# Performance work log

Measured on AMD Instinct MI355X. Metric: run time of the kernel, lower is better.

## Reference

```python
import jax, jax.numpy as jnp
import numpy as np

B, C, HEADS, W, Hh = 8, 512, 8, 32, 32
D = C // HEADS  # 64 per-head dim
N = W * Hh      # 1024 spatial tokens


def setup_inputs() -> dict:
    key = jax.random.key(0)
    ks = jax.random.split(key, 10)
    s = 1.0 / np.sqrt(C)
    return {
        "x": jax.random.normal(ks[0], (B, C, W, Hh), dtype=jnp.float32),
        "Wq": jax.random.normal(ks[1], (C, C), dtype=jnp.float32) * s,
        "bq": jax.random.normal(ks[2], (C,), dtype=jnp.float32) * 0.01,
        "Wk": jax.random.normal(ks[3], (C, C), dtype=jnp.float32) * s,
        "bk": jax.random.normal(ks[4], (C,), dtype=jnp.float32) * 0.01,
        "Wv": jax.random.normal(ks[5], (C, C), dtype=jnp.float32) * s,
        "bv": jax.random.normal(ks[6], (C,), dtype=jnp.float32) * 0.01,
        "rel_h": jax.random.normal(ks[7], (1, HEADS, D, 1, Hh), dtype=jnp.float32),
        "rel_w": jax.random.normal(ks[8], (1, HEADS, D, W, 1), dtype=jnp.float32),
    }


def reference(x, Wq, bq, Wk, bk, Wv, bv, rel_h, rel_w):
    b = x.shape[0]
    xf = x.reshape(b, C, N)  # [B, C, N] — 1x1 conv == per-position linear
    proj = lambda Wm, bm: (jnp.einsum('oc,bcn->bon', Wm, xf) + bm[None, :, None]).reshape(b, HEADS, D, N)
    q = proj(Wq, bq)  # [B, H, D, N]
    k = proj(Wk, bk)
    v = proj(Wv, bv)
    # content-content: q^T k -> [B, H, N, N]
    cc = jnp.einsum('bhdn,bhdm->bhnm', q, k)
    # relative position bias: (rel_h + rel_w) -> [H, D, N], then rel^T @ q
    rel = (rel_h + rel_w).reshape(HEADS, D, N)
    cp = jnp.einsum('hdn,bhdm->bhnm', rel, q)  # [B, H, N, N]
    attn = jax.nn.softmax(cc + cp, axis=-1)
    # out = v @ attn^T : out[d,m] = sum_n v[d,n] * attn[m,n]
    out = jnp.einsum('bhdn,bhmn->bhdm', v, attn)  # [B, H, D, N]
    return out.reshape(b, C, W, Hh)
```

## Files before the change

kernel.cpp:

```cpp
#include <hip/hip_runtime.h>

typedef _Float16 half8 __attribute__((ext_vector_type(8)));
typedef _Float16 half4 __attribute__((ext_vector_type(4)));
typedef float f32x4 __attribute__((ext_vector_type(4)));

__device__ __forceinline__ void glds16(const void* g, void* l) {
    __builtin_amdgcn_global_load_lds(
        (const __attribute__((address_space(1))) unsigned int*)g,
        (__attribute__((address_space(3))) unsigned int*)l, 16, 0, 0);
}


__global__ void k_prep_all(const float* __restrict__ Wq, const float* __restrict__ Wk,
                           const float* __restrict__ Wv, const float* __restrict__ bq,
                           const float* __restrict__ bk, const float* __restrict__ bv,
                           const float* __restrict__ x, const float* __restrict__ rel_h,
                           const float* __restrict__ rel_w, _Float16* __restrict__ Wf,
                           float* __restrict__ bias2, _Float16* __restrict__ xTf,
                           _Float16* __restrict__ rel2) {
    __shared__ float xs[64][65];
    int bid = blockIdx.x;
    if (bid < 384) {
        int t = bid * 256 + threadIdx.x;
        int m = t >> 6;
        int c8 = (t & 63) << 3;
        const float* src = (m < 512) ? (Wq + m * 512)
                         : (m < 1024 ? (Wk + (m - 512) * 512) : (Wv + (m - 1024) * 512));
        float4 v0 = *(const float4*)(src + c8);
        float4 v1 = *(const float4*)(src + c8 + 4);
        half8 o;
        o[0] = (_Float16)v0.x; o[1] = (_Float16)v0.y; o[2] = (_Float16)v0.z; o[3] = (_Float16)v0.w;
        o[4] = (_Float16)v1.x; o[5] = (_Float16)v1.y; o[6] = (_Float16)v1.z; o[7] = (_Float16)v1.w;
        *(half8*)(Wf + (size_t)m * 512 + c8) = o;
        if (t < 1536)
            bias2[t] = (t < 512) ? bq[t] : (t < 1024 ? bk[t - 512] : bv[t - 1024]);
    } else if (bid < 1408) {
        int i = bid - 384;
        int nt = (i & 15) << 6, ct = ((i >> 4) & 7) << 6, b = i >> 7;
        int t = threadIdx.x;
        const float* xb = x + ((size_t)b * 512 + ct) * 1024 + nt;
#pragma unroll
        for (int p = 0; p < 4; ++p) {
            int c = p * 16 + (t >> 4), n4 = (t & 15) * 4;
            float4 v = *(const float4*)(xb + (size_t)c * 1024 + n4);
            xs[c][n4] = v.x; xs[c][n4 + 1] = v.y; xs[c][n4 + 2] = v.z; xs[c][n4 + 3] = v.w;
        }
        __syncthreads();
        int nl = t >> 2, part = t & 3;
        _Float16* rowp = xTf + ((size_t)b * 1024 + nt + nl) * 512;
#pragma unroll
        for (int g = 0; g < 2; ++g) {
            half8 o;
#pragma unroll
            for (int j = 0; j < 8; ++j)
                o[j] = (_Float16)xs[part * 16 + g * 8 + j][nl];
            *(half8*)(rowp + ct + part * 16 + g * 8) = o;
        }
    } else {
        int tid = (bid - 1408) * 256 + threadIdx.x;
        int h = tid >> 13;
        int rem = tid & 8191;
        int n = rem >> 3;
        int g = rem & 7;
        int hh = n & 31, ww = n >> 5;
        half8 o;
#pragma unroll
        for (int j = 0; j < 8; ++j) {
            int d = g * 8 + j;
            o[j] = (_Float16)(rel_h[(h * 64 + d) * 32 + hh] + rel_w[(h * 64 + d) * 32 + ww]);
        }
        *(half8*)(rel2 + ((size_t)h * 1024 + n) * 64 + g * 8) = o;
    }
}

__global__ __launch_bounds__(256, 3) void k_proj(const _Float16* __restrict__ Wf,
                                                 const _Float16* __restrict__ xTf,
                                                 const float* __restrict__ bias2,
                                                 _Float16* __restrict__ q2,
                                                 _Float16* __restrict__ k2,
                                                 _Float16* __restrict__ vb) {
    __shared__ __align__(16) _Float16 As[8192];
    __shared__ __align__(16) _Float16 Bs[8192];
    int t = threadIdx.x;
    int lane = t & 63, w = t >> 6;
    int lm = lane & 15, lq = lane >> 4;
    int wr = (w >> 1) * 64, wc = (w & 1) * 64;
    int mb = blockIdx.y * 128, nb = blockIdx.x * 128, b = blockIdx.z;
    int rl = lane >> 2;
    int csw = ((lane & 3) ^ ((lane >> 3) & 3)) * 8;
    const _Float16* Ag0 = Wf + (size_t)(mb + w * 32 + rl) * 512 + csw;
    const _Float16* Ag1 = Ag0 + 16 * 512;
    const _Float16* Bg0 = xTf + ((size_t)b * 1024 + nb + w * 32 + rl) * 512 + csw;
    const _Float16* Bg1 = Bg0 + 16 * 512;
    f32x4 acc[4][4];
#pragma unroll
    for (int i = 0; i < 4; ++i)
#pragma unroll
        for (int j = 0; j < 4; ++j) acc[i][j] = {0.f, 0.f, 0.f, 0.f};
    int fsw = (lq ^ ((lm >> 1) & 3)) * 8;
    for (int k0 = 0; k0 < 512; k0 += 64) {
#pragma unroll
        for (int kh = 0; kh < 2; ++kh) {
            int ko = k0 + kh * 32;
            glds16(Ag0 + ko, &As[kh * 4096 + (w * 32) * 32]);
            glds16(Ag1 + ko, &As[kh * 4096 + (w * 32 + 16) * 32]);
            glds16(Bg0 + ko, &Bs[kh * 4096 + (w * 32) * 32]);
            glds16(Bg1 + ko, &Bs[kh * 4096 + (w * 32 + 16) * 32]);
        }
        __syncthreads();
#pragma unroll
        for (int kh = 0; kh < 2; ++kh) {
            half8 af[4], bfr[4];
#pragma unroll
            for (int mt = 0; mt < 4; ++mt)
                af[mt] = *(half8*)&As[kh * 4096 + (wr + mt * 16 + lm) * 32 + fsw];
#pragma unroll
            for (int nt = 0; nt < 4; ++nt)
                bfr[nt] = *(half8*)&Bs[kh * 4096 + (wc + nt * 16 + lm) * 32 + fsw];
#pragma unroll
            for (int mt = 0; mt < 4; ++mt)
#pragma unroll
                for (int nt = 0; nt < 4; ++nt)
                    acc[mt][nt] = __builtin_amdgcn_mfma_f32_16x16x32_f16(af[mt], bfr[nt], acc[mt][nt], 0, 0, 0);
        }
        __syncthreads();
    }
    int sect = mb >> 9;
    int hloc = ((mb & 511) + wr) >> 6;
    size_t bh = (size_t)b * 8 + hloc;
    if (sect < 2) {
        float sc = (sect == 0) ? 1.44269504089f : 1.0f;
        _Float16* dst = (sect == 0 ? q2 : k2) + bh * 1024 * 64;
#pragma unroll
        for (int mt = 0; mt < 4; ++mt) {
            int d0 = mt * 16 + lq * 4;
            float bi0 = bias2[mb + wr + d0];
            float bi1 = bias2[mb + wr + d0 + 1];
            float bi2 = bias2[mb + wr + d0 + 2];
            float bi3 = bias2[mb + wr + d0 + 3];
#pragma unroll
            for (int nt = 0; nt < 4; ++nt) {
                int n = nb + wc + nt * 16 + lm;
                half4 o;
                o[0] = (_Float16)((acc[mt][nt][0] + bi0) * sc);
                o[1] = (_Float16)((acc[mt][nt][1] + bi1) * sc);
                o[2] = (_Float16)((acc[mt][nt][2] + bi2) * sc);
                o[3] = (_Float16)((acc[mt][nt][3] + bi3) * sc);
                *(half4*)(dst + (size_t)n * 64 + d0) = o;
            }
        }
    } else {
        _Float16* dst = vb + bh * 64 * 1024;
#pragma unroll
        for (int mt = 0; mt < 4; ++mt)
#pragma unroll
            for (int reg = 0; reg < 4; ++reg) {
                int d = mt * 16 + lq * 4 + reg;
                float bi = bias2[mb + wr + d];
#pragma unroll
                for (int nt = 0; nt < 4; ++nt) {
                    int n = nb + wc + nt * 16 + lm;
                    dst[(size_t)d * 1024 + n] = (_Float16)(acc[mt][nt][reg] + bi);
                }
            }
    }
}

__global__ __launch_bounds__(256, 3) void k_attn(const _Float16* __restrict__ q2,
                                                 const _Float16* __restrict__ k2,
                                                 const _Float16* __restrict__ rel2,
                                                 const _Float16* __restrict__ vb,
                                                 float* __restrict__ out) {
    __shared__ __align__(16) char pool[45056];
    _Float16* kb_s = (_Float16*)pool;
    _Float16* v_s  = (_Float16*)(pool + 17408);
    _Float16* p_s  = (_Float16*)(pool + 26624);
    int t = threadIdx.x;
    int lane = t & 63, w = t >> 6;
    int lm = lane & 15, lq = lane >> 4;
    int lin = blockIdx.x;
    int mt0 = lin >> 6;
    int bh_ = lin & 63;
    int h = bh_ & 7, b = bh_ >> 3;
    size_t bh = (size_t)b * 8 + h;
    const _Float16* q2b = q2 + bh * 1024 * 64;
    const _Float16* k2b = k2 + bh * 1024 * 64;
    const _Float16* relb = rel2 + (size_t)h * 1024 * 64;
    const _Float16* vbb = vb + bh * 64 * 1024;
    float* outb = out + bh * 64 * 1024 + mt0 * 128;

    int r = t >> 2, part = t & 3;
    const _Float16* ksrc = ((part < 2) ? (k2b + part * 32) : (q2b + (part - 2) * 32));
    int vc = (t & 3) * 16;
    const _Float16* vsrcb = vbb + (size_t)r * 1024 + vc;
    _Float16* kdst = kb_s + r * 136 + part * 32;
    _Float16* vdst = v_s + r * 72 + vc;

    uint4 kc0, kc1, kc2, kc3, vv0, vv1;
    {
        const uint4* s_ = (const uint4*)(ksrc + (size_t)r * 64);
        kc0 = s_[0]; kc1 = s_[1]; kc2 = s_[2]; kc3 = s_[3];
        const uint4* v_ = (const uint4*)vsrcb;
        vv0 = v_[0]; vv1 = v_[1];
    }

    {
        int n = mt0 * 128 + r;
        const _Float16* src = (part < 2) ? (q2b + (size_t)n * 64 + part * 32)
                                         : (relb + (size_t)n * 64 + (part - 2) * 32);
        ((uint4*)kdst)[0] = ((const uint4*)src)[0];
        ((uint4*)kdst)[1] = ((const uint4*)src)[1];
        ((uint4*)kdst)[2] = ((const uint4*)src)[2];
        ((uint4*)kdst)[3] = ((const uint4*)src)[3];
    }
    __syncthreads();
    half8 ah0[4], ah1[4];
#pragma unroll
    for (int kk = 0; kk < 4; ++kk)
        ah0[kk] = *(half8*)&kb_s[(w * 16 + lm) * 136 + kk * 32 + lq * 8];
    __syncthreads();
    {
        int n = mt0 * 128 + 64 + r;
        const _Float16* src = (part < 2) ? (q2b + (size_t)n * 64 + part * 32)
                                         : (relb + (size_t)n * 64 + (part - 2) * 32);
        ((uint4*)kdst)[0] = ((const uint4*)src)[0];
        ((uint4*)kdst)[1] = ((const uint4*)src)[1];
        ((uint4*)kdst)[2] = ((const uint4*)src)[2];
        ((uint4*)kdst)[3] = ((const uint4*)src)[3];
    }
    __syncthreads();
#pragma unroll
    for (int kk = 0; kk < 4; ++kk)
        ah1[kk] = *(half8*)&kb_s[(w * 16 + lm) * 136 + kk * 32 + lq * 8];
    __syncthreads();

    f32x4 acco0[4], acco1[4];
#pragma unroll
    for (int i = 0; i < 4; ++i) { acco0[i] = {0.f, 0.f, 0.f, 0.f}; acco1[i] = {0.f, 0.f, 0.f, 0.f}; }
    float mrun0 = -3e38f, lrun0 = 0.f, mrun1 = -3e38f, lrun1 = 0.f;

    for (int kt = 0; kt < 16; ++kt) {
        ((uint4*)kdst)[0] = kc0;
        ((uint4*)kdst)[1] = kc1;
        ((uint4*)kdst)[2] = kc2;
        ((uint4*)kdst)[3] = kc3;
        ((uint4*)vdst)[0] = vv0;
        ((uint4*)vdst)[1] = vv1;
        __syncthreads();
        int nn = ((kt + 1) & 15) * 64;
        const uint4* s_ = (const uint4*)(ksrc + (size_t)(nn + r) * 64);
        uint4 kn0 = s_[0], kn1 = s_[1], kn2 = s_[2], kn3 = s_[3];
        const uint4* v_ = (const uint4*)(vsrcb + nn);
        uint4 vn0 = v_[0], vn1 = v_[1];
        f32x4 s0[4], s1[4];
#pragma unroll
        for (int ct = 0; ct < 4; ++ct) { s0[ct] = {0.f, 0.f, 0.f, 0.f}; s1[ct] = {0.f, 0.f, 0.f, 0.f}; }
#pragma unroll
        for (int ct = 0; ct < 4; ++ct) {
            half8 kf[4];
#pragma unroll
            for (int kk = 0; kk < 4; ++kk)
                kf[kk] = *(half8*)&kb_s[(ct * 16 + lm) * 136 + kk * 32 + lq * 8];
#pragma unroll
            for (int kk = 0; kk < 4; ++kk) {
                s0[ct] = __builtin_amdgcn_mfma_f32_16x16x32_f16(kf[kk], ah0[kk], s0[ct], 0, 0, 0);
                s1[ct] = __builtin_amdgcn_mfma_f32_16x16x32_f16(kf[kk], ah1[kk], s1[ct], 0, 0, 0);
            }
        }
        {
            float mx = -3e38f;
#pragma unroll
            for (int ct = 0; ct < 4; ++ct)
#pragma unroll
                for (int reg = 0; reg < 4; ++reg) mx = fmaxf(mx, s0[ct][reg]);
            mx = fmaxf(mx, __shfl_xor(mx, 16));
            mx = fmaxf(mx, __shfl_xor(mx, 32));
            float mnew = fmaxf(mrun0, mx);
            float al_ = exp2f(mrun0 - mnew);
            float rs = 0.f;
#pragma unroll
            for (int ct = 0; ct < 4; ++ct) {
                float p0 = exp2f(s0[ct][0] - mnew);
                float p1 = exp2f(s0[ct][1] - mnew);
                float p2 = exp2f(s0[ct][2] - mnew);
                float p3 = exp2f(s0[ct][3] - mnew);
                rs += (p0 + p1) + (p2 + p3);
                half4 o; o[0] = (_Float16)p0; o[1] = (_Float16)p1; o[2] = (_Float16)p2; o[3] = (_Float16)p3;
                *(half4*)&p_s[(w * 16 + lm) * 72 + ct * 16 + lq * 4] = o;
            }
            rs += __shfl_xor(rs, 16);
            rs += __shfl_xor(rs, 32);
            lrun0 = lrun0 * al_ + rs;
            mrun0 = mnew;
#pragma unroll
            for (int dt = 0; dt < 4; ++dt) {
                acco0[dt][0] *= al_; acco0[dt][1] *= al_;
                acco0[dt][2] *= al_; acco0[dt][3] *= al_;
            }
        }
        {
            float mx = -3e38f;
#pragma unroll
            for (int ct = 0; ct < 4; ++ct)
#pragma unroll
                for (int reg = 0; reg < 4; ++reg) mx = fmaxf(mx, s1[ct][reg]);
            mx = fmaxf(mx, __shfl_xor(mx, 16));
            mx = fmaxf(mx, __shfl_xor(mx, 32));
            float mnew = fmaxf(mrun1, mx);
            float al_ = exp2f(mrun1 - mnew);
            float rs = 0.f;
#pragma unroll
            for (int ct = 0; ct < 4; ++ct) {
                float p0 = exp2f(s1[ct][0] - mnew);
                float p1 = exp2f(s1[ct][1] - mnew);
                float p2 = exp2f(s1[ct][2] - mnew);
                float p3 = exp2f(s1[ct][3] - mnew);
                rs += (p0 + p1) + (p2 + p3);
                half4 o; o[0] = (_Float16)p0; o[1] = (_Float16)p1; o[2] = (_Float16)p2; o[3] = (_Float16)p3;
                *(half4*)&p_s[(64 + w * 16 + lm) * 72 + ct * 16 + lq * 4] = o;
            }
            rs += __shfl_xor(rs, 16);
            rs += __shfl_xor(rs, 32);
            lrun1 = lrun1 * al_ + rs;
            mrun1 = mnew;
#pragma unroll
            for (int dt = 0; dt < 4; ++dt) {
                acco1[dt][0] *= al_; acco1[dt][1] *= al_;
                acco1[dt][2] *= al_; acco1[dt][3] *= al_;
            }
        }
        half8 p0f[2], p1f[2];
#pragma unroll
        for (int ch = 0; ch < 2; ++ch) {
            p0f[ch] = *(half8*)&p_s[(w * 16 + lm) * 72 + ch * 32 + lq * 8];
            p1f[ch] = *(half8*)&p_s[(64 + w * 16 + lm) * 72 + ch * 32 + lq * 8];
        }
#pragma unroll
        for (int dt = 0; dt < 4; ++dt) {
            half8 vf0 = *(half8*)&v_s[(dt * 16 + lm) * 72 + lq * 8];
            half8 vf1 = *(half8*)&v_s[(dt * 16 + lm) * 72 + 32 + lq * 8];
            acco0[dt] = __builtin_amdgcn_mfma_f32_16x16x32_f16(vf0, p0f[0], acco0[dt], 0, 0, 0);
            acco0[dt] = __builtin_amdgcn_mfma_f32_16x16x32_f16(vf1, p0f[1], acco0[dt], 0, 0, 0);
            acco1[dt] = __builtin_amdgcn_mfma_f32_16x16x32_f16(vf0, p1f[0], acco1[dt], 0, 0, 0);
            acco1[dt] = __builtin_amdgcn_mfma_f32_16x16x32_f16(vf1, p1f[1], acco1[dt], 0, 0, 0);
        }
        __syncthreads();
        kc0 = kn0; kc1 = kn1; kc2 = kn2; kc3 = kn3;
        vv0 = vn0; vv1 = vn1;
    }
    float li0 = 1.f / lrun0, li1 = 1.f / lrun1;
#pragma unroll
    for (int dt = 0; dt < 4; ++dt)
#pragma unroll
        for (int reg = 0; reg < 4; ++reg) {
            int d = dt * 16 + lq * 4 + reg;
            outb[(size_t)d * 1024 + w * 16 + lm] = acco0[dt][reg] * li0;
            outb[(size_t)d * 1024 + 64 + w * 16 + lm] = acco1[dt][reg] * li1;
        }
}

extern "C" void kernel_launch(void* const* d_in, const int* in_sizes, int n_in,
                              void* d_out, int out_size, void* d_ws, size_t ws_size,
                              hipStream_t stream) {
    const float* x     = (const float*)d_in[0];
    const float* Wq    = (const float*)d_in[1];
    const float* bq    = (const float*)d_in[2];
    const float* Wk    = (const float*)d_in[3];
    const float* bk    = (const float*)d_in[4];
    const float* Wv    = (const float*)d_in[5];
    const float* bv    = (const float*)d_in[6];
    const float* rel_h = (const float*)d_in[7];
    const float* rel_w = (const float*)d_in[8];
    char* ws = (char*)d_ws;
    _Float16* Wf   = (_Float16*)(ws);
    float* bias2   = (float*)(ws + 1572864);
    _Float16* xTf  = (_Float16*)(ws + 1579008);
    _Float16* q2   = (_Float16*)(ws + 9967616);
    _Float16* k2   = (_Float16*)(ws + 18356224);
    _Float16* vb   = (_Float16*)(ws + 26744832);
    _Float16* rel2 = (_Float16*)(ws + 35133440);
    float* out = (float*)d_out;

    hipLaunchKernelGGL(k_prep_all, dim3(1664),     dim3(256), 0, stream,
                       Wq, Wk, Wv, bq, bk, bv, x, rel_h, rel_w, Wf, bias2, xTf, rel2);
    hipLaunchKernelGGL(k_proj,     dim3(8, 12, 8), dim3(256), 0, stream, Wf, xTf, bias2, q2, k2, vb);
    hipLaunchKernelGGL(k_attn,     dim3(512),      dim3(256), 0, stream, q2, k2, rel2, vb, out);
}
```

Baseline: 153.6 us.

## Swizzle attention LDS tiles, add lazy softmax rescale, setprio and packed conversion

Replaces the padded LDS layouts for the K/Q, V and P tiles with XOR-swizzled unpadded rows, aiming to avoid bank conflicts while shrinking shared memory. Online softmax now rescales the accumulators only when the row max grows by more than a threshold, which skips most rescale multiplies. MFMA sections are wrapped in s_setprio, and probabilities are converted with the packed round-toward-zero instruction. The lazy rescale lets unnormalised values grow up to 2^8 before rescaling, which is a small fp16 precision and overflow risk.

```diff
diff --git a/kernel.cpp b/kernel.cpp
--- a/kernel.cpp
+++ b/kernel.cpp
@@ -2,6 +2,7 @@
 
 typedef _Float16 half8 __attribute__((ext_vector_type(8)));
 typedef _Float16 half4 __attribute__((ext_vector_type(4)));
+typedef __fp16 fp16x2 __attribute__((ext_vector_type(2)));
 typedef float f32x4 __attribute__((ext_vector_type(4)));
 
 __device__ __forceinline__ void glds16(const void* g, void* l) {
@@ -171,10 +172,10 @@
                                                  const _Float16* __restrict__ rel2,
                                                  const _Float16* __restrict__ vb,
                                                  float* __restrict__ out) {
-    __shared__ __align__(16) char pool[45056];
-    _Float16* kb_s = (_Float16*)pool;
-    _Float16* v_s  = (_Float16*)(pool + 17408);
-    _Float16* p_s  = (_Float16*)(pool + 26624);
+    __shared__ __align__(16) char pool[40960];
+    char* kb_s = pool;
+    char* v_s  = pool + 16384;
+    char* p_s  = pool + 24576;
     int t = threadIdx.x;
     int lane = t & 63, w = t >> 6;
     int lm = lane & 15, lq = lane >> 4;
@@ -190,11 +191,12 @@
     float* outb = out + bh * 64 * 1024 + mt0 * 128;
 
     int r = t >> 2, part = t & 3;
+    int wsw = (r & 7) << 4;
+    int rsw = (lm & 7) << 4;
     const _Float16* ksrc = ((part < 2) ? (k2b + part * 32) : (q2b + (part - 2) * 32));
-    int vc = (t & 3) * 16;
-    const _Float16* vsrcb = vbb + (size_t)r * 1024 + vc;
-    _Float16* kdst = kb_s + r * 136 + part * 32;
-    _Float16* vdst = v_s + r * 72 + vc;
+    const _Float16* vsrcb = vbb + (size_t)r * 1024 + part * 16;
+    char* kdst = kb_s + r * 256;
+    char* vdst = v_s + r * 128;
 
     uint4 kc0, kc1, kc2, kc3, vv0, vv1;
     {
@@ -208,30 +210,30 @@
         int n = mt0 * 128 + r;
         const _Float16* src = (part < 2) ? (q2b + (size_t)n * 64 + part * 32)
                                          : (relb + (size_t)n * 64 + (part - 2) * 32);
-        ((uint4*)kdst)[0] = ((const uint4*)src)[0];
-        ((uint4*)kdst)[1] = ((const uint4*)src)[1];
-        ((uint4*)kdst)[2] = ((const uint4*)src)[2];
-        ((uint4*)kdst)[3] = ((const uint4*)src)[3];
+        *(uint4*)(kdst + ((part * 64 +  0) ^ wsw)) = ((const uint4*)src)[0];
+        *(uint4*)(kdst + ((part * 64 + 16) ^ wsw)) = ((const uint4*)src)[1];
+        *(uint4*)(kdst + ((part * 64 + 32) ^ wsw)) = ((const uint4*)src)[2];
+        *(uint4*)(kdst + ((part * 64 + 48) ^ wsw)) = ((const uint4*)src)[3];
     }
     __syncthreads();
     half8 ah0[4], ah1[4];
 #pragma unroll
     for (int kk = 0; kk < 4; ++kk)
-        ah0[kk] = *(half8*)&kb_s[(w * 16 + lm) * 136 + kk * 32 + lq * 8];
+        ah0[kk] = *(half8*)(kb_s + (w * 16 + lm) * 256 + ((kk * 64 + lq * 16) ^ rsw));
     __syncthreads();
     {
         int n = mt0 * 128 + 64 + r;
         const _Float16* src = (part < 2) ? (q2b + (size_t)n * 64 + part * 32)
                                          : (relb + (size_t)n * 64 + (part - 2) * 32);
-        ((uint4*)kdst)[0] = ((const uint4*)src)[0];
-        ((uint4*)kdst)[1] = ((const uint4*)src)[1];
-        ((uint4*)kdst)[2] = ((const uint4*)src)[2];
-        ((uint4*)kdst)[3] = ((const uint4*)src)[3];
+        *(uint4*)(kdst + ((part * 64 +  0) ^ wsw)) = ((const uint4*)src)[0];
+        *(uint4*)(kdst + ((part * 64 + 16) ^ wsw)) = ((const uint4*)src)[1];
+        *(uint4*)(kdst + ((part * 64 + 32) ^ wsw)) = ((const uint4*)src)[2];
+        *(uint4*)(kdst + ((part * 64 + 48) ^ wsw)) = ((const uint4*)src)[3];
     }
     __syncthreads();
 #pragma unroll
     for (int kk = 0; kk < 4; ++kk)
-        ah1[kk] = *(half8*)&kb_s[(w * 16 + lm) * 136 + kk * 32 + lq * 8];
+        ah1[kk] = *(half8*)(kb_s + (w * 16 + lm) * 256 + ((kk * 64 + lq * 16) ^ rsw));
     __syncthreads();
 
     f32x4 acco0[4], acco1[4];
@@ -240,12 +242,12 @@
     float mrun0 = -3e38f, lrun0 = 0.f, mrun1 = -3e38f, lrun1 = 0.f;
 
     for (int kt = 0; kt < 16; ++kt) {
-        ((uint4*)kdst)[0] = kc0;
-        ((uint4*)kdst)[1] = kc1;
-        ((uint4*)kdst)[2] = kc2;
-        ((uint4*)kdst)[3] = kc3;
-        ((uint4*)vdst)[0] = vv0;
-        ((uint4*)vdst)[1] = vv1;
+        *(uint4*)(kdst + ((part * 64 +  0) ^ wsw)) = kc0;
+        *(uint4*)(kdst + ((part * 64 + 16) ^ wsw)) = kc1;
+        *(uint4*)(kdst + ((part * 64 + 32) ^ wsw)) = kc2;
+        *(uint4*)(kdst + ((part * 64 + 48) ^ wsw)) = kc3;
+        *(uint4*)(vdst + ((part * 32 +  0) ^ wsw)) = vv0;
+        *(uint4*)(vdst + ((part * 32 + 16) ^ wsw)) = vv1;
         __syncthreads();
         int nn = ((kt + 1) & 15) * 64;
         const uint4* s_ = (const uint4*)(ksrc + (size_t)(nn + r) * 64);
@@ -255,95 +257,119 @@
         f32x4 s0[4], s1[4];
 #pragma unroll
         for (int ct = 0; ct < 4; ++ct) { s0[ct] = {0.f, 0.f, 0.f, 0.f}; s1[ct] = {0.f, 0.f, 0.f, 0.f}; }
+        __builtin_amdgcn_s_setprio(1);
 #pragma unroll
         for (int ct = 0; ct < 4; ++ct) {
             half8 kf[4];
 #pragma unroll
             for (int kk = 0; kk < 4; ++kk)
-                kf[kk] = *(half8*)&kb_s[(ct * 16 + lm) * 136 + kk * 32 + lq * 8];
+                kf[kk] = *(half8*)(kb_s + (ct * 16 + lm) * 256 + ((kk * 64 + lq * 16) ^ rsw));
 #pragma unroll
             for (int kk = 0; kk < 4; ++kk) {
                 s0[ct] = __builtin_amdgcn_mfma_f32_16x16x32_f16(kf[kk], ah0[kk], s0[ct], 0, 0, 0);
                 s1[ct] = __builtin_amdgcn_mfma_f32_16x16x32_f16(kf[kk], ah1[kk], s1[ct], 0, 0, 0);
             }
         }
+        __builtin_amdgcn_s_setprio(0);
         {
             float mx = -3e38f;
 #pragma unroll
-            for (int ct = 0; ct < 4; ++ct)
-#pragma unroll
-                for (int reg = 0; reg < 4; ++reg) mx = fmaxf(mx, s0[ct][reg]);
+            for (int ct = 0; ct < 4; ++ct) {
+                float a_ = fmaxf(s0[ct][0], s0[ct][1]);
+                float b2 = fmaxf(s0[ct][2], s0[ct][3]);
+                mx = fmaxf(mx, fmaxf(a_, b2));
+            }
             mx = fmaxf(mx, __shfl_xor(mx, 16));
             mx = fmaxf(mx, __shfl_xor(mx, 32));
-            float mnew = fmaxf(mrun0, mx);
-            float al_ = exp2f(mrun0 - mnew);
+            if (__any(mx > mrun0 + 8.f)) {
+                float mnew = fmaxf(mrun0, mx);
+                float al_ = exp2f(mrun0 - mnew);
+                lrun0 *= al_;
+#pragma unroll
+                for (int dt = 0; dt < 4; ++dt) {
+                    acco0[dt][0] *= al_; acco0[dt][1] *= al_;
+                    acco0[dt][2] *= al_; acco0[dt][3] *= al_;
+                }
+                mrun0 = mnew;
+            }
             float rs = 0.f;
+            char* prow = p_s + (w * 16 + lm) * 128;
 #pragma unroll
             for (int ct = 0; ct < 4; ++ct) {
-                float p0 = exp2f(s0[ct][0] - mnew);
-                float p1 = exp2f(s0[ct][1] - mnew);
-                float p2 = exp2f(s0[ct][2] - mnew);
-                float p3 = exp2f(s0[ct][3] - mnew);
+                float p0 = exp2f(s0[ct][0] - mrun0);
+                float p1 = exp2f(s0[ct][1] - mrun0);
+                float p2 = exp2f(s0[ct][2] - mrun0);
+                float p3 = exp2f(s0[ct][3] - mrun0);
                 rs += (p0 + p1) + (p2 + p3);
-                half4 o; o[0] = (_Float16)p0; o[1] = (_Float16)p1; o[2] = (_Float16)p2; o[3] = (_Float16)p3;
-                *(half4*)&p_s[(w * 16 + lm) * 72 + ct * 16 + lq * 4] = o;
+                fp16x2 lo = __builtin_amdgcn_cvt_pkrtz(p0, p1);
+                fp16x2 hi = __builtin_amdgcn_cvt_pkrtz(p2, p3);
+                uint2 pk;
+                pk.x = __builtin_bit_cast(unsigned int, lo);
+                pk.y = __builtin_bit_cast(unsigned int, hi);
+                *(uint2*)(prow + ((ct * 32 + lq * 8) ^ rsw)) = pk;
             }
             rs += __shfl_xor(rs, 16);
             rs += __shfl_xor(rs, 32);
-            lrun0 = lrun0 * al_ + rs;
-            mrun0 = mnew;
-#pragma unroll
-            for (int dt = 0; dt < 4; ++dt) {
-                acco0[dt][0] *= al_; acco0[dt][1] *= al_;
-                acco0[dt][2] *= al_; acco0[dt][3] *= al_;
-            }
+            lrun0 += rs;
         }
         {
             float mx = -3e38f;
 #pragma unroll
-            for (int ct = 0; ct < 4; ++ct)
-#pragma unroll
-                for (int reg = 0; reg < 4; ++reg) mx = fmaxf(mx, s1[ct][reg]);
+            for (int ct = 0; ct < 4; ++ct) {
+                float a_ = fmaxf(s1[ct][0], s1[ct][1]);
+                float b2 = fmaxf(s1[ct][2], s1[ct][3]);
+                mx = fmaxf(mx, fmaxf(a_, b2));
+            }
             mx = fmaxf(mx, __shfl_xor(mx, 16));
             mx = fmaxf(mx, __shfl_xor(mx, 32));
-            float mnew = fmaxf(mrun1, mx);
-            float al_ = exp2f(mrun1 - mnew);
+            if (__any(mx > mrun1 + 8.f)) {
+                float mnew = fmaxf(mrun1, mx);
+                float al_ = exp2f(mrun1 - mnew);
+                lrun1 *= al_;
+#pragma unroll
+                for (int dt = 0; dt < 4; ++dt) {
+                    acco1[dt][0] *= al_; acco1[dt][1] *= al_;
+                    acco1[dt][2] *= al_; acco1[dt][3] *= al_;
+                }
+                mrun1 = mnew;
+            }
             float rs = 0.f;
+            char* prow = p_s + (64 + w * 16 + lm) * 128;
 #pragma unroll
             for (int ct = 0; ct < 4; ++ct) {
-                float p0 = exp2f(s1[ct][0] - mnew);
-                float p1 = exp2f(s1[ct][1] - mnew);
-                float p2 = exp2f(s1[ct][2] - mnew);
-                float p3 = exp2f(s1[ct][3] - mnew);
+                float p0 = exp2f(s1[ct][0] - mrun1);
+                float p1 = exp2f(s1[ct][1] - mrun1);
+                float p2 = exp2f(s1[ct][2] - mrun1);
+                float p3 = exp2f(s1[ct][3] - mrun1);
                 rs += (p0 + p1) + (p2 + p3);
-                half4 o; o[0] = (_Float16)p0; o[1] = (_Float16)p1; o[2] = (_Float16)p2; o[3] = (_Float16)p3;
-                *(half4*)&p_s[(64 + w * 16 + lm) * 72 + ct * 16 + lq * 4] = o;
+                fp16x2 lo = __builtin_amdgcn_cvt_pkrtz(p0, p1);
+                fp16x2 hi = __builtin_amdgcn_cvt_pkrtz(p2, p3);
+                uint2 pk;
+                pk.x = __builtin_bit_cast(unsigned int, lo);
+                pk.y = __builtin_bit_cast(unsigned int, hi);
+                *(uint2*)(prow + ((ct * 32 + lq * 8) ^ rsw)) = pk;
             }
             rs += __shfl_xor(rs, 16);
             rs += __shfl_xor(rs, 32);
-            lrun1 = lrun1 * al_ + rs;
-            mrun1 = mnew;
-#pragma unroll
-            for (int dt = 0; dt < 4; ++dt) {
-                acco1[dt][0] *= al_; acco1[dt][1] *= al_;
-                acco1[dt][2] *= al_; acco1[dt][3] *= al_;
-            }
+            lrun1 += rs;
         }
         half8 p0f[2], p1f[2];
 #pragma unroll
         for (int ch = 0; ch < 2; ++ch) {
-            p0f[ch] = *(half8*)&p_s[(w * 16 + lm) * 72 + ch * 32 + lq * 8];
-            p1f[ch] = *(half8*)&p_s[(64 + w * 16 + lm) * 72 + ch * 32 + lq * 8];
-        }
+            p0f[ch] = *(half8*)(p_s + (w * 16 + lm) * 128 + ((ch * 64 + lq * 16) ^ rsw));
+            p1f[ch] = *(half8*)(p_s + (64 + w * 16 + lm) * 128 + ((ch * 64 + lq * 16) ^ rsw));
+        }
+        __builtin_amdgcn_s_setprio(1);
 #pragma unroll
         for (int dt = 0; dt < 4; ++dt) {
-            half8 vf0 = *(half8*)&v_s[(dt * 16 + lm) * 72 + lq * 8];
-            half8 vf1 = *(half8*)&v_s[(dt * 16 + lm) * 72 + 32 + lq * 8];
+            half8 vf0 = *(half8*)(v_s + (dt * 16 + lm) * 128 + ((lq * 16) ^ rsw));
+            half8 vf1 = *(half8*)(v_s + (dt * 16 + lm) * 128 + ((64 + lq * 16) ^ rsw));
             acco0[dt] = __builtin_amdgcn_mfma_f32_16x16x32_f16(vf0, p0f[0], acco0[dt], 0, 0, 0);
             acco0[dt] = __builtin_amdgcn_mfma_f32_16x16x32_f16(vf1, p0f[1], acco0[dt], 0, 0, 0);
             acco1[dt] = __builtin_amdgcn_mfma_f32_16x16x32_f16(vf0, p1f[0], acco1[dt], 0, 0, 0);
             acco1[dt] = __builtin_amdgcn_mfma_f32_16x16x32_f16(vf1, p1f[1], acco1[dt], 0, 0, 0);
         }
+        __builtin_amdgcn_s_setprio(0);
         __syncthreads();
         kc0 = kn0; kc1 = kn1; kc2 = kn2; kc3 = kn3;
         vv0 = vn0; vv1 = vn1;
```

Result: no change. 152.5 us (-0.7%).
